# Kernel optimization log

Hardware: AMD Instinct MI355X
Metric: run time of the kernel (lower is better)

Reference implementation:

```python
import jax, jax.numpy as jnp
import numpy as np

NEG = jnp.float32(-1e30)  # log(0) surrogate


def _ctc_loss(logits, labels, label_lengths):
    """CTC loss matching tf.nn.ctc_loss semantics: softmax applied internally,
    blank index = last class, full logit_length = T, mean over batch.

    logits: [B, T, C] float, labels: [B, L] int (padded), label_lengths: [B] int.
    """
    B, T, C = logits.shape
    blank = C - 1
    logp = jax.nn.log_softmax(logits.astype(jnp.float32), axis=-1)  # [B,T,C]
    L = labels.shape[1]
    S = 2 * L + 1  # extended label: blank, l1, blank, l2, ..., blank

    ext = jnp.full((B, S), blank, dtype=jnp.int32).at[:, 1::2].set(labels.astype(jnp.int32))
    # emission log-probs per extended position: [B, T, S]
    emit = jnp.take_along_axis(logp, jnp.broadcast_to(ext[:, None, :], (B, T, S)), axis=2)

    # skip transition s-2 -> s allowed iff ext[s] is a label differing from ext[s-2]
    prev2 = jnp.pad(ext[:, :-2], ((0, 0), (2, 0)), constant_values=-1)
    allow2 = (ext != blank) & (ext != prev2)  # [B,S]

    ll = label_lengths.astype(jnp.int32)
    valid = jnp.arange(S)[None, :] < (2 * ll[:, None] + 1)  # [B,S]

    # t = 0: only s=0 (blank) and s=1 (first label) reachable
    alpha0 = jnp.full((B, S), NEG)
    alpha0 = alpha0.at[:, 0].set(0.0)
    alpha0 = alpha0.at[:, 1].set(jnp.where(ll > 0, 0.0, NEG))
    alpha0 = jnp.where(valid, alpha0 + emit[:, 0, :], NEG)

    def step(alpha, emit_t):
        s1 = jnp.pad(alpha[:, :-1], ((0, 0), (1, 0)), constant_values=NEG)
        s2 = jnp.pad(alpha[:, :-2], ((0, 0), (2, 0)), constant_values=NEG)
        s2 = jnp.where(allow2, s2, NEG)
        a = jax.scipy.special.logsumexp(jnp.stack([alpha, s1, s2]), axis=0) + emit_t
        a = jnp.where(valid, a, NEG)
        return a, None

    alpha, _ = jax.lax.scan(step, alpha0, jnp.swapaxes(emit, 0, 1)[1:])  # scan over T-1 steps

    # terminate at final blank (s=2*ll) or final label (s=2*ll-1)
    a_end1 = jnp.take_along_axis(alpha, (2 * ll)[:, None], axis=1)[:, 0]
    a_end2 = jnp.take_along_axis(alpha, jnp.maximum(2 * ll - 1, 0)[:, None], axis=1)[:, 0]
    a_end2 = jnp.where(ll > 0, a_end2, NEG)
    loss = -jnp.logaddexp(a_end1, a_end2)  # [B]
    return jnp.mean(loss)


def setup_inputs() -> dict:
    key = jax.random.key(0)
    k1, k2, k3 = jax.random.split(key, 3)
    B, T, L, C = 32, 1024, 128, 801  # C = num_classes + 1 (blank = 800)
    logits = jax.random.normal(k1, (B, T, C), dtype=jnp.float32)
    labels = jax.random.randint(k2, (B, L), 0, 800, dtype=jnp.int32)
    label_lengths = jax.random.randint(k3, (B,), 64, L + 1, dtype=jnp.int32)
    return {"logits": logits, "labels": labels, "label_lengths": label_lengths}


def reference(logits, labels, label_lengths):
    return _ctc_loss(logits, labels, label_lengths)
```

## Files before the change

### kernel.cpp

```cpp
#include <hip/hip_runtime.h>
#include <math.h>

#define B_ 32
#define T_ 1024
#define C_ 801
#define L_ 128
#define S_ 257
#define BLANK 800
#define NEGV -1e30f

#define CH 128
#define NCH (T_ / CH)
#define NW 8
#define LN2F 0.69314718055994531f

typedef const unsigned __attribute__((address_space(1))) u32_g;
typedef unsigned __attribute__((address_space(3))) u32_l;

template <int CTRL>
__device__ __forceinline__ float dppf(float v) {
    return __uint_as_float((unsigned)__builtin_amdgcn_update_dpp(
        0, (int)__float_as_uint(v), CTRL, 0xf, 0xf, true));
}
__device__ __forceinline__ float shift_up1(float v) { return dppf<0x138>(v); }

__device__ __forceinline__ float wave_red_max63(float v) {
    v = fmaxf(v, dppf<0xB1>(v));
    v = fmaxf(v, dppf<0x4E>(v));
    v = fmaxf(v, dppf<0x141>(v));
    v = fmaxf(v, dppf<0x140>(v));
    v = fmaxf(v, dppf<0x142>(v));
    v = fmaxf(v, dppf<0x143>(v));
    return v;
}
__device__ __forceinline__ float wave_red_sum63(float v) {
    v += dppf<0xB1>(v);
    v += dppf<0x4E>(v);
    v += dppf<0x141>(v);
    v += dppf<0x140>(v);
    v += dppf<0x142>(v);
    v += dppf<0x143>(v);
    return v;
}
__device__ __forceinline__ float bcast63(float v) {
    return __uint_as_float((unsigned)__builtin_amdgcn_readlane((int)__float_as_uint(v), 63));
}
__device__ __forceinline__ float wave_max_nn(float v) { return bcast63(wave_red_max63(v)); }

__device__ __forceinline__ float bf16lo(unsigned u) { return __uint_as_float(u << 16); }
__device__ __forceinline__ float bf16hi(unsigned u) { return __uint_as_float(u & 0xFFFF0000u); }
__device__ __forceinline__ unsigned short f32_to_bf16_rne(float f) {
    unsigned u = __float_as_uint(f);
    u += 0x7FFF + ((u >> 16) & 1);
    return (unsigned short)(u >> 16);
}

#define RLANE(x, j) __uint_as_float((unsigned)__builtin_amdgcn_readlane((int)__float_as_uint(x), (j)))

__device__ __forceinline__ float tree_max13(const float* v) {
    float a = fmaxf(v[0], v[1]), b = fmaxf(v[2], v[3]), c = fmaxf(v[4], v[5]);
    float d = fmaxf(v[6], v[7]), e = fmaxf(v[8], v[9]), f = fmaxf(v[10], v[11]);
    return fmaxf(fmaxf(fmaxf(a, b), fmaxf(c, d)), fmaxf(fmaxf(e, f), v[12]));
}
__device__ __forceinline__ float tree_expsum13(const float* v, float m) {
    float e0 = __expf(v[0] - m),  e1 = __expf(v[1] - m),  e2 = __expf(v[2] - m);
    float e3 = __expf(v[3] - m),  e4 = __expf(v[4] - m),  e5 = __expf(v[5] - m);
    float e6 = __expf(v[6] - m),  e7 = __expf(v[7] - m),  e8 = __expf(v[8] - m);
    float e9 = __expf(v[9] - m),  eA = __expf(v[10] - m), eB = __expf(v[11] - m);
    float eC = __expf(v[12] - m);
    float a = (e0 + e1) + (e2 + e3), b = (e4 + e5) + (e6 + e7), c = (e8 + e9) + (eA + eB);
    return (a + b) + (c + eC);
}

__global__ __launch_bounds__(256) void stage_kernel(const float* __restrict__ logits,
                                                    const int* __restrict__ labels,
                                                    const int* __restrict__ lens,
                                                    unsigned* __restrict__ ea32,
                                                    float* __restrict__ ebq) {
    const int tid = threadIdx.x, lane = tid & 63, wv = tid >> 6;
    const int b = blockIdx.y;
    const int t0 = blockIdx.x * 8;
    const float* __restrict__ base = logits + ((size_t)b * T_ + t0) * C_;
    __shared__ float xs[8 * C_];

    const float4* src = (const float4*)base;
    #pragma unroll
    for (int k = 0; k < 7; ++k) {
        int idx = tid + 256 * k;
        if (idx < 1602) ((float4*)xs)[idx] = src[idx];
    }
    __syncthreads();

    const float* xrA = xs + (2 * wv) * C_;
    const float* xrB = xrA + C_;

    float vA[13], vB[13];
    #pragma unroll
    for (int k = 0; k < 12; ++k) { vA[k] = xrA[lane + 64 * k]; vB[k] = xrB[lane + 64 * k]; }
    vA[12] = (lane < 33) ? xrA[768 + lane] : NEGV;
    vB[12] = (lane < 33) ? xrB[768 + lane] : NEGV;

    float mA = bcast63(wave_red_max63(tree_max13(vA)));
    float mB = bcast63(wave_red_max63(tree_max13(vB)));
    float sA = bcast63(wave_red_sum63(tree_expsum13(vA, mA)));
    float sB = bcast63(wave_red_sum63(tree_expsum13(vB, mB)));
    const float lseA = mA + __logf(sA);
    const float lseB = mB + __logf(sB);

    const int ll = lens[b];
    const int il1 = labels[b * L_ + 2 * lane];
    const int il3 = labels[b * L_ + 2 * lane + 1];
    const bool k1 = (2 * lane < ll), k3 = (2 * lane + 1 < ll);

    const int rowA = b * T_ + t0 + 2 * wv;

    float e1A = k1 ? __expf(xrA[il1] - lseA) * 1024.0f : 0.f;
    float e3A = k3 ? __expf(xrA[il3] - lseA) * 1024.0f : 0.f;
    float e1B = k1 ? __expf(xrB[il1] - lseB) * 1024.0f : 0.f;
    float e3B = k3 ? __expf(xrB[il3] - lseB) * 1024.0f : 0.f;

    unsigned packA = ((unsigned)f32_to_bf16_rne(e3A) << 16) | (unsigned)f32_to_bf16_rne(e1A);
    unsigned packB = ((unsigned)f32_to_bf16_rne(e3B) << 16) | (unsigned)f32_to_bf16_rne(e1B);
    ea32[(size_t)rowA * 64 + lane] = packA;
    ea32[(size_t)(rowA + 1) * 64 + lane] = packB;

    if (lane == 0) {
        float2 eb;
        eb.x = __expf(xrA[BLANK] - lseA) * 1024.0f;
        eb.y = __expf(xrB[BLANK] - lseB) * 1024.0f;
        *(float2*)(ebq + rowA) = eb;
    }
}


__device__ __forceinline__ void stage_chunk_split(const unsigned* gbase, int c,
                                                  unsigned* lbase, int lane, int wid) {
    #pragma unroll
    for (int k = 0; k < CH / NW; ++k) {
        int r = wid + k * NW;
        const unsigned* gp = gbase + ((size_t)(c * CH + r)) * 64 + lane;
        unsigned* lp = lbase + r * 64;
        __builtin_amdgcn_global_load_lds((u32_g*)gp, (u32_l*)lp, 4, 0, 0);
    }
}

template <int FIRST>
__device__ __forceinline__ void compute_chunk(const unsigned* bufp, float ebv0, float ebv1,
                                              int lane, float m21, float m23,
                                              float mask0, float mask2, float kq,
                                              float& p0, float& p1, float& p2, float& p3,
                                              float& q, int& E) {
    #pragma unroll
    for (int g = 0; g < CH / 8; ++g) {
        unsigned u[8];
        #pragma unroll
        for (int k = 0; k < 8; ++k) u[k] = bufp[(g * 8 + k) * 64 + lane];
        #pragma unroll
        for (int k = 0; k < 8; ++k) {
            if (FIRST && g == 0 && k == 0) continue;
            const int j = g * 8 + k;
            float ebt = (j < 64) ? RLANE(ebv0, j) : RLANE(ebv1, j - 64);
            float el0 = bf16lo(u[k]);
            float el1 = bf16hi(u[k]);
            float ebm0 = ebt * mask0;
            float ebm2 = ebt * mask2;
            float eqm  = ebt * kq;
            float shp3 = shift_up1(p3);
            float n0 = (p0 + shp3) * ebm0;
            float n1 = fmaf(m21, shp3, p1 + p0) * el0;
            float n2 = (p2 + p1) * ebm2;
            float n3 = fmaf(m23, p1, p3 + p2) * el1;
            q = (q + p3) * eqm;
            p0 = n0; p1 = n1; p2 = n2; p3 = n3;
        }
        float mx = fmaxf(fmaxf(p0, p1), fmaxf(p2, fmaxf(p3, q)));
        mx = wave_max_nn(mx);
        int e2_ = (int)((__float_as_uint(mx) >> 23) & 0xFF) - 126;
        float sc_ = __uint_as_float((unsigned)(127 - e2_) << 23);
        p0 *= sc_; p1 *= sc_; p2 *= sc_; p3 *= sc_; q *= sc_;
        E += e2_;
    }
}

__global__ __launch_bounds__(NW * 64) void ctc_lds_kernel(const unsigned* __restrict__ ea32,
                                                          const float* __restrict__ ebq,
                                                          const int* __restrict__ labels,
                                                          const int* __restrict__ lens,
                                                          float* __restrict__ loss) {
    __shared__ unsigned buf[2][CH * 64];
    const int b = blockIdx.x;
    const int tid = threadIdx.x;
    const int lane = tid & 63;
    const int wid = tid >> 6;
    const int ll = lens[b];
    const unsigned* gbase = ea32 + (size_t)b * T_ * 64;
    const float* qb = ebq + b * T_;

    float m21 = 0.f, m23 = 0.f, mask0 = 0.f, mask2 = 0.f, kq = 0.f;
    if (wid == 0) {
        int s1 = 4 * lane + 1;
        if (s1 >= 3) {
            int li = s1 >> 1;
            m21 = (labels[b * L_ + li] != labels[b * L_ + li - 1]) ? 1.f : 0.f;
        }
        int li3 = (4 * lane + 3) >> 1;
        m23 = (labels[b * L_ + li3] != labels[b * L_ + li3 - 1]) ? 1.f : 0.f;
        const int smax = 2 * ll + 1;
        mask0 = (4 * lane     < smax) ? 1.f : 0.f;
        mask2 = (4 * lane + 2 < smax) ? 1.f : 0.f;
        kq    = (ll == 128) ? 1.f : 0.f;
    }

    stage_chunk_split(gbase, 0, buf[0], lane, wid);
    float ebv0 = 0.f, ebv1 = 0.f, ebn0 = 0.f, ebn1 = 0.f;
    if (wid == 0) { ebv0 = qb[lane]; ebv1 = qb[64 + lane]; }
    __syncthreads();

    float p0 = 0.f, p1 = 0.f, p2 = 0.f, p3 = 0.f, q = 0.f;
    if (wid == 0) {
        float eb0 = RLANE(ebv0, 0);
        unsigned w0 = buf[0][lane];
        p0 = (lane == 0) ? eb0 : 0.f;
        p1 = (lane == 0) ? bf16lo(w0) : 0.f;
    }
    int E = 0;

    #pragma unroll 1
    for (int c = 0; c < NCH; ++c) {
        if (c + 1 < NCH) {
            stage_chunk_split(gbase, c + 1, buf[(c + 1) & 1], lane, wid);
            if (wid == 0) { ebn0 = qb[(c + 1) * CH + lane]; ebn1 = qb[(c + 1) * CH + 64 + lane]; }
        }
        if (wid == 0) {
            if (c == 0) compute_chunk<1>(buf[0],     ebv0, ebv1, lane, m21, m23,
                                         mask0, mask2, kq, p0, p1, p2, p3, q, E);
            else        compute_chunk<0>(buf[c & 1], ebv0, ebv1, lane, m21, m23,
                                         mask0, mask2, kq, p0, p1, p2, p3, q, E);
            ebv0 = ebn0; ebv1 = ebn1;
        }
        __syncthreads();
    }

    float* pf = (float*)(&buf[0][0]);
    if (wid == 0) {
        *(float4*)(pf + 4 * lane) = make_float4(p0, p1, p2, p3);
        if (lane == 63) pf[256] = q;
    }
    __syncthreads();
    if (tid == 0) {
        float a1 = pf[2 * ll];
        float a2 = (ll > 0) ? pf[2 * ll - 1] : 0.f;
        loss[b] = -(__logf(a1 + a2) + ((float)E - 10240.0f) * LN2F);
    }
}

__global__ void mean_kernel(const float* __restrict__ loss, float* __restrict__ out) {
    if (threadIdx.x == 0) {
        float s = 0.f;
        for (int i = 0; i < B_; ++i) s += loss[i];
        out[0] = s / (float)B_;
    }
}


__global__ __launch_bounds__(256) void lse_kernel(const float* __restrict__ logits,
                                                  float* __restrict__ lse) {
    const int row = blockIdx.x;
    const float* __restrict__ x = logits + (size_t)row * C_;
    const int tid = threadIdx.x, lane = tid & 63, wid = tid >> 6;
    float v0 = x[tid], v1 = x[tid + 256], v2 = x[tid + 512];
    bool h3 = (tid + 768) < C_;
    float v3 = h3 ? x[tid + 768] : NEGV;
    float m = fmaxf(fmaxf(v0, v1), fmaxf(v2, v3));
    #pragma unroll
    for (int off = 32; off > 0; off >>= 1) m = fmaxf(m, __shfl_down(m, off));
    __shared__ float wred[4]; __shared__ float bm;
    if (lane == 0) wred[wid] = m;
    __syncthreads();
    if (tid == 0) bm = fmaxf(fmaxf(wred[0], wred[1]), fmaxf(wred[2], wred[3]));
    __syncthreads();
    m = bm;
    float s = __expf(v0 - m) + __expf(v1 - m) + __expf(v2 - m);
    if (h3) s += __expf(v3 - m);
    #pragma unroll
    for (int off = 32; off > 0; off >>= 1) s += __shfl_down(s, off);
    __syncthreads();
    if (lane == 0) wred[wid] = s;
    __syncthreads();
    if (tid == 0) lse[row] = m + __logf(wred[0] + wred[1] + wred[2] + wred[3]);
}

__global__ __launch_bounds__(320) void ctc_alpha_kernel(const float* __restrict__ logits,
                                                        const int* __restrict__ labels,
                                                        const int* __restrict__ lens,
                                                        const float* __restrict__ lse,
                                                        float* __restrict__ loss) {
    const int b = blockIdx.x;
    const int s = threadIdx.x;
    const int ll = lens[b];
    __shared__ float albuf[2][S_ + 2];
    if (s < 2) { albuf[0][s] = NEGV; albuf[1][s] = NEGV; }
    int cls = BLANK; bool allow2 = false;
    if (s < S_ && (s & 1)) {
        cls = labels[b * L_ + (s >> 1)];
        allow2 = (s >= 3) && (cls != labels[b * L_ + (s >> 1) - 1]);
    }
    const bool valid = (s < 2 * ll + 1);
    const float* __restrict__ xb = logits + (size_t)b * T_ * C_;
    const float* __restrict__ lseb = lse + b * T_;
    if (s < S_) {
        float e0 = xb[cls] - lseb[0];
        float a = (s == 0 || (s == 1 && ll > 0)) ? e0 : NEGV;
        if (!valid) a = NEGV;
        albuf[0][2 + s] = a;
    }
    __syncthreads();
    float e_next = xb[(size_t)C_ + cls];
    float lse_next = lseb[1];
    int cur = 0;
    for (int t = 1; t < T_; ++t) {
        const float e = e_next, lse_t = lse_next;
        if (t + 1 < T_) { e_next = xb[(size_t)(t + 1) * C_ + cls]; lse_next = lseb[t + 1]; }
        if (s < S_) {
            float a0 = albuf[cur][2 + s];
            float a1 = albuf[cur][1 + s];
            float a2 = allow2 ? albuf[cur][s] : NEGV;
            float m = fmaxf(fmaxf(a0, a1), a2);
            float r = m + __logf(__expf(a0 - m) + __expf(a1 - m) + __expf(a2 - m)) + (e - lse_t);
            if (!valid) r = NEGV;
            albuf[cur ^ 1][2 + s] = r;
        }
        __syncthreads();
        cur ^= 1;
    }
    if (s == 0) {
        float a1 = albuf[cur][2 + 2 * ll];
        float a2 = (ll > 0) ? albuf[cur][2 + 2 * ll - 1] : NEGV;
        float m = fmaxf(a1, a2);
        loss[b] = -(m + __logf(__expf(a1 - m) + __expf(a2 - m)));
    }
}


extern "C" void kernel_launch(void* const* d_in, const int* in_sizes, int n_in,
                              void* d_out, int out_size, void* d_ws, size_t ws_size,
                              hipStream_t stream) {
    const float* logits = (const float*)d_in[0];
    const int*   labels = (const int*)d_in[1];
    const int*   lens   = (const int*)d_in[2];
    float* out = (float*)d_out;

    const size_t ea_elems = (size_t)B_ * T_ * 64;
    const size_t eb_elems = (size_t)B_ * T_;
    const size_t need = (ea_elems + eb_elems + B_) * 4;

    if (ws_size >= need) {
        unsigned* ea32 = (unsigned*)d_ws;
        float* ebq  = (float*)(ea32 + ea_elems);
        float* loss = ebq + eb_elems;
        dim3 grid(T_ / 8, B_);
        stage_kernel<<<grid, 256, 0, stream>>>(logits, labels, lens, ea32, ebq);
        ctc_lds_kernel<<<B_, NW * 64, 0, stream>>>(ea32, ebq, labels, lens, loss);
        mean_kernel<<<1, 64, 0, stream>>>(loss, out);
    } else {
        float* lse  = (float*)d_ws;
        float* loss = lse + (size_t)B_ * T_;
        lse_kernel<<<B_ * T_, 256, 0, stream>>>(logits, lse);
        ctc_alpha_kernel<<<B_, 320, 0, stream>>>(logits, labels, lens, lse, loss);
        mean_kernel<<<1, 64, 0, stream>>>(loss, out);
    }
}
```

Before: 74.60 us.

## Fuse log-softmax staging into the CTC recurrence kernel with producer warps

Removes the separate stage kernel and its global intermediate buffers. Each batch now runs in one 1024-thread block: 15 producer waves read logits rows, compute log-sum-exp and the emission probabilities, and write them into double-buffered LDS. Wave 0 runs the alpha recurrence on the previous chunk at the same time. This saves a kernel launch and the global write and re-read of the staged data, but only 32 blocks now have to stream the whole 105 MB of logits, so bandwidth may be limited by low parallelism.

Result: slower. 112.0 us (+50.2%).

```diff
diff --git a/kernel.cpp b/kernel.cpp
--- a/kernel.cpp
+++ b/kernel.cpp
@@ -11,11 +11,8 @@
 
 #define CH 128
 #define NCH (T_ / CH)
-#define NW 8
+#define NWF 16
 #define LN2F 0.69314718055994531f
-
-typedef const unsigned __attribute__((address_space(1))) u32_g;
-typedef unsigned __attribute__((address_space(3))) u32_l;
 
 template <int CTRL>
 __device__ __forceinline__ float dppf(float v) {
@@ -72,129 +69,56 @@
     return (a + b) + (c + eC);
 }
 
-__global__ __launch_bounds__(256) void stage_kernel(const float* __restrict__ logits,
-                                                    const int* __restrict__ labels,
-                                                    const int* __restrict__ lens,
-                                                    unsigned* __restrict__ ea32,
-                                                    float* __restrict__ ebq) {
-    const int tid = threadIdx.x, lane = tid & 63, wv = tid >> 6;
-    const int b = blockIdx.y;
-    const int t0 = blockIdx.x * 8;
-    const float* __restrict__ base = logits + ((size_t)b * T_ + t0) * C_;
-    __shared__ float xs[8 * C_];
-
-    const float4* src = (const float4*)base;
-    #pragma unroll
-    for (int k = 0; k < 7; ++k) {
-        int idx = tid + 256 * k;
-        if (idx < 1602) ((float4*)xs)[idx] = src[idx];
-    }
-    __syncthreads();
-
-    const float* xrA = xs + (2 * wv) * C_;
-    const float* xrB = xrA + C_;
-
-    float vA[13], vB[13];
-    #pragma unroll
-    for (int k = 0; k < 12; ++k) { vA[k] = xrA[lane + 64 * k]; vB[k] = xrB[lane + 64 * k]; }
-    vA[12] = (lane < 33) ? xrA[768 + lane] : NEGV;
-    vB[12] = (lane < 33) ? xrB[768 + lane] : NEGV;
-
-    float mA = bcast63(wave_red_max63(tree_max13(vA)));
-    float mB = bcast63(wave_red_max63(tree_max13(vB)));
-    float sA = bcast63(wave_red_sum63(tree_expsum13(vA, mA)));
-    float sB = bcast63(wave_red_sum63(tree_expsum13(vB, mB)));
-    const float lseA = mA + __logf(sA);
-    const float lseB = mB + __logf(sB);
-
-    const int ll = lens[b];
-    const int il1 = labels[b * L_ + 2 * lane];
-    const int il3 = labels[b * L_ + 2 * lane + 1];
-    const bool k1 = (2 * lane < ll), k3 = (2 * lane + 1 < ll);
-
-    const int rowA = b * T_ + t0 + 2 * wv;
-
-    float e1A = k1 ? __expf(xrA[il1] - lseA) * 1024.0f : 0.f;
-    float e3A = k3 ? __expf(xrA[il3] - lseA) * 1024.0f : 0.f;
-    float e1B = k1 ? __expf(xrB[il1] - lseB) * 1024.0f : 0.f;
-    float e3B = k3 ? __expf(xrB[il3] - lseB) * 1024.0f : 0.f;
-
-    unsigned packA = ((unsigned)f32_to_bf16_rne(e3A) << 16) | (unsigned)f32_to_bf16_rne(e1A);
-    unsigned packB = ((unsigned)f32_to_bf16_rne(e3B) << 16) | (unsigned)f32_to_bf16_rne(e1B);
-    ea32[(size_t)rowA * 64 + lane] = packA;
-    ea32[(size_t)(rowA + 1) * 64 + lane] = packB;
-
-    if (lane == 0) {
-        float2 eb;
-        eb.x = __expf(xrA[BLANK] - lseA) * 1024.0f;
-        eb.y = __expf(xrB[BLANK] - lseB) * 1024.0f;
-        *(float2*)(ebq + rowA) = eb;
-    }
-}
-
-
-__device__ __forceinline__ void stage_chunk_split(const unsigned* gbase, int c,
-                                                  unsigned* lbase, int lane, int wid) {
-    #pragma unroll
-    for (int k = 0; k < CH / NW; ++k) {
-        int r = wid + k * NW;
-        const unsigned* gp = gbase + ((size_t)(c * CH + r)) * 64 + lane;
-        unsigned* lp = lbase + r * 64;
-        __builtin_amdgcn_global_load_lds((u32_g*)gp, (u32_l*)lp, 4, 0, 0);
-    }
-}
-
-template <int FIRST>
-__device__ __forceinline__ void compute_chunk(const unsigned* bufp, float ebv0, float ebv1,
-                                              int lane, float m21, float m23,
-                                              float mask0, float mask2, float kq,
-                                              float& p0, float& p1, float& p2, float& p3,
-                                              float& q, int& E) {
-    #pragma unroll
-    for (int g = 0; g < CH / 8; ++g) {
-        unsigned u[8];
-        #pragma unroll
-        for (int k = 0; k < 8; ++k) u[k] = bufp[(g * 8 + k) * 64 + lane];
-        #pragma unroll
-        for (int k = 0; k < 8; ++k) {
-            if (FIRST && g == 0 && k == 0) continue;
-            const int j = g * 8 + k;
-            float ebt = (j < 64) ? RLANE(ebv0, j) : RLANE(ebv1, j - 64);
-            float el0 = bf16lo(u[k]);
-            float el1 = bf16hi(u[k]);
-            float ebm0 = ebt * mask0;
-            float ebm2 = ebt * mask2;
-            float eqm  = ebt * kq;
-            float shp3 = shift_up1(p3);
-            float n0 = (p0 + shp3) * ebm0;
-            float n1 = fmaf(m21, shp3, p1 + p0) * el0;
-            float n2 = (p2 + p1) * ebm2;
-            float n3 = fmaf(m23, p1, p3 + p2) * el1;
-            q = (q + p3) * eqm;
-            p0 = n0; p1 = n1; p2 = n2; p3 = n3;
-        }
-        float mx = fmaxf(fmaxf(p0, p1), fmaxf(p2, fmaxf(p3, q)));
-        mx = wave_max_nn(mx);
-        int e2_ = (int)((__float_as_uint(mx) >> 23) & 0xFF) - 126;
-        float sc_ = __uint_as_float((unsigned)(127 - e2_) << 23);
-        p0 *= sc_; p1 *= sc_; p2 *= sc_; p3 *= sc_; q *= sc_;
-        E += e2_;
-    }
-}
-
-__global__ __launch_bounds__(NW * 64) void ctc_lds_kernel(const unsigned* __restrict__ ea32,
-                                                          const float* __restrict__ ebq,
-                                                          const int* __restrict__ labels,
-                                                          const int* __restrict__ lens,
-                                                          float* __restrict__ loss) {
-    __shared__ unsigned buf[2][CH * 64];
+__global__ __launch_bounds__(NWF * 64) void ctc_fused_kernel(const float* __restrict__ logits,
+                                                             const int* __restrict__ labels,
+                                                             const int* __restrict__ lens,
+                                                             float* __restrict__ loss) {
+    __shared__ unsigned ebuf[2][CH * 64];
+    __shared__ float    bbuf[2][CH];
+
     const int b = blockIdx.x;
     const int tid = threadIdx.x;
     const int lane = tid & 63;
     const int wid = tid >> 6;
     const int ll = lens[b];
-    const unsigned* gbase = ea32 + (size_t)b * T_ * 64;
-    const float* qb = ebq + b * T_;
+    const float* __restrict__ xb = logits + (size_t)b * T_ * C_;
+
+    const int il1 = labels[b * L_ + 2 * lane];
+    const int il3 = labels[b * L_ + 2 * lane + 1];
+    const bool k1 = (2 * lane < ll), k3 = (2 * lane + 1 < ll);
+
+    struct Row { float v[13]; float g1, g3; };
+    auto load_row = [&](int t, Row& R) {
+        const float* x = xb + (size_t)t * C_;
+        #pragma unroll
+        for (int k = 0; k < 12; ++k) R.v[k] = x[lane + 64 * k];
+        R.v[12] = (lane < 33) ? x[768 + lane] : NEGV;
+        R.g1 = x[il1];
+        R.g3 = x[il3];
+    };
+    auto emit_row = [&](int r, int sb, const Row& R) {
+        float m = bcast63(wave_red_max63(tree_max13(R.v)));
+        float s = bcast63(wave_red_sum63(tree_expsum13(R.v, m)));
+        float lse = m + __logf(s);
+        float e1 = k1 ? __expf(R.g1 - lse) * 1024.0f : 0.f;
+        float e3 = k3 ? __expf(R.g3 - lse) * 1024.0f : 0.f;
+        unsigned pack = ((unsigned)f32_to_bf16_rne(e3) << 16) | (unsigned)f32_to_bf16_rne(e1);
+        ebuf[sb][r * 64 + lane] = pack;
+        float blg = RLANE(R.v[12], 32);
+        if (lane == 0) bbuf[sb][r] = __expf(blg - lse) * 1024.0f;
+    };
+    auto stage_chunk = [&](int cc, int sb) {
+        int r = wid - 1;
+        Row cur, nxt;
+        if (r < CH) load_row(cc * CH + r, cur);
+        while (r < CH) {
+            int rn = r + 15;
+            if (rn < CH) load_row(cc * CH + rn, nxt);
+            emit_row(r, sb, cur);
+            cur = nxt;
+            r = rn;
+        }
+    };
 
     float m21 = 0.f, m23 = 0.f, mask0 = 0.f, mask2 = 0.f, kq = 0.f;
     if (wid == 0) {
@@ -211,37 +135,62 @@
         kq    = (ll == 128) ? 1.f : 0.f;
     }
 
-    stage_chunk_split(gbase, 0, buf[0], lane, wid);
-    float ebv0 = 0.f, ebv1 = 0.f, ebn0 = 0.f, ebn1 = 0.f;
-    if (wid == 0) { ebv0 = qb[lane]; ebv1 = qb[64 + lane]; }
+    if (wid > 0) stage_chunk(0, 0);
     __syncthreads();
 
     float p0 = 0.f, p1 = 0.f, p2 = 0.f, p3 = 0.f, q = 0.f;
     if (wid == 0) {
-        float eb0 = RLANE(ebv0, 0);
-        unsigned w0 = buf[0][lane];
+        unsigned w0 = ebuf[0][lane];
+        float eb0 = bbuf[0][0];
         p0 = (lane == 0) ? eb0 : 0.f;
         p1 = (lane == 0) ? bf16lo(w0) : 0.f;
     }
     int E = 0;
 
     #pragma unroll 1
-    for (int c = 0; c < NCH; ++c) {
-        if (c + 1 < NCH) {
-            stage_chunk_split(gbase, c + 1, buf[(c + 1) & 1], lane, wid);
-            if (wid == 0) { ebn0 = qb[(c + 1) * CH + lane]; ebn1 = qb[(c + 1) * CH + 64 + lane]; }
-        }
-        if (wid == 0) {
-            if (c == 0) compute_chunk<1>(buf[0],     ebv0, ebv1, lane, m21, m23,
-                                         mask0, mask2, kq, p0, p1, p2, p3, q, E);
-            else        compute_chunk<0>(buf[c & 1], ebv0, ebv1, lane, m21, m23,
-                                         mask0, mask2, kq, p0, p1, p2, p3, q, E);
-            ebv0 = ebn0; ebv1 = ebn1;
+    for (int cc = 0; cc < NCH; ++cc) {
+        const int cs = cc & 1;
+        if (wid > 0) {
+            if (cc + 1 < NCH) stage_chunk(cc + 1, cs ^ 1);
+        } else {
+            float ebv0 = bbuf[cs][lane];
+            float ebv1 = bbuf[cs][64 + lane];
+            const unsigned* bufp = ebuf[cs];
+            #pragma unroll
+            for (int g = 0; g < CH / 8; ++g) {
+                unsigned u[8];
+                #pragma unroll
+                for (int k = 0; k < 8; ++k) u[k] = bufp[(g * 8 + k) * 64 + lane];
+                #pragma unroll
+                for (int k = 0; k < 8; ++k) {
+                    if (cc == 0 && g == 0 && k == 0) continue;
+                    const int j = g * 8 + k;
+                    float ebt = (j < 64) ? RLANE(ebv0, j) : RLANE(ebv1, j - 64);
+                    float el0 = bf16lo(u[k]);
+                    float el1 = bf16hi(u[k]);
+                    float ebm0 = ebt * mask0;
+                    float ebm2 = ebt * mask2;
+                    float eqm  = ebt * kq;
+                    float shp3 = shift_up1(p3);
+                    float n0 = (p0 + shp3) * ebm0;
+                    float n1 = fmaf(m21, shp3, p1 + p0) * el0;
+                    float n2 = (p2 + p1) * ebm2;
+                    float n3 = fmaf(m23, p1, p3 + p2) * el1;
+                    q = (q + p3) * eqm;
+                    p0 = n0; p1 = n1; p2 = n2; p3 = n3;
+                }
+                float mx = fmaxf(fmaxf(p0, p1), fmaxf(p2, fmaxf(p3, q)));
+                mx = wave_max_nn(mx);
+                int e2_ = (int)((__float_as_uint(mx) >> 23) & 0xFF) - 126;
+                float sc_ = __uint_as_float((unsigned)(127 - e2_) << 23);
+                p0 *= sc_; p1 *= sc_; p2 *= sc_; p3 *= sc_; q *= sc_;
+                E += e2_;
+            }
         }
         __syncthreads();
     }
 
-    float* pf = (float*)(&buf[0][0]);
+    float* pf = (float*)(&ebuf[0][0]);
     if (wid == 0) {
         *(float4*)(pf + 4 * lane) = make_float4(p0, p1, p2, p3);
         if (lane == 63) pf[256] = q;
@@ -350,17 +299,9 @@
     const int*   lens   = (const int*)d_in[2];
     float* out = (float*)d_out;
 
-    const size_t ea_elems = (size_t)B_ * T_ * 64;
-    const size_t eb_elems = (size_t)B_ * T_;
-    const size_t need = (ea_elems + eb_elems + B_) * 4;
-
-    if (ws_size >= need) {
-        unsigned* ea32 = (unsigned*)d_ws;
-        float* ebq  = (float*)(ea32 + ea_elems);
-        float* loss = ebq + eb_elems;
-        dim3 grid(T_ / 8, B_);
-        stage_kernel<<<grid, 256, 0, stream>>>(logits, labels, lens, ea32, ebq);
-        ctc_lds_kernel<<<B_, NW * 64, 0, stream>>>(ea32, ebq, labels, lens, loss);
+    if (ws_size >= (size_t)B_ * sizeof(float)) {
+        float* loss = (float*)d_ws;
+        ctc_fused_kernel<<<B_, NWF * 64, 0, stream>>>(logits, labels, lens, loss);
         mean_kernel<<<1, 64, 0, stream>>>(loss, out);
     } else {
         float* lse  = (float*)d_ws;
```
